# Performance work log

Measured on AMD Instinct MI355X. Metric: run time of the kernel, lower is better.

## Reference

```python
import jax, jax.numpy as jnp
import numpy as np

EMBED_DIM = 1024
NUM_HEADS = 16
HEAD_DIM = EMBED_DIM // NUM_HEADS
SPARSITY_LAMBDA = 0.01
B, S = 2, 2048


def setup_inputs() -> dict:
    key = jax.random.key(0)
    ks = jax.random.split(key, 10)
    scale = 0.02
    inp = {
        "x": jax.random.normal(ks[0], (B, S, EMBED_DIM), dtype=jnp.float32),
        "Wq": jax.random.normal(ks[1], (EMBED_DIM, EMBED_DIM), dtype=jnp.float32) * scale,
        "bq": jnp.zeros((EMBED_DIM,), dtype=jnp.float32),
        "Wk": jax.random.normal(ks[2], (EMBED_DIM, EMBED_DIM), dtype=jnp.float32) * scale,
        "bk": jnp.zeros((EMBED_DIM,), dtype=jnp.float32),
        "Wv": jax.random.normal(ks[3], (EMBED_DIM, EMBED_DIM), dtype=jnp.float32) * scale,
        "bv": jnp.zeros((EMBED_DIM,), dtype=jnp.float32),
        "Wo": jax.random.normal(ks[4], (EMBED_DIM, EMBED_DIM), dtype=jnp.float32) * scale,
        "bo": jnp.zeros((EMBED_DIM,), dtype=jnp.float32),
        "z": jax.random.normal(ks[5], (NUM_HEADS,), dtype=jnp.float32),
    }
    return inp


def reference(x, Wq, bq, Wk, bk, Wv, bv, Wo, bo, z):
    # Linear layers (torch Linear: y = x @ W.T + b); W here stored as [out, in]
    def split_heads(t):  # [B,S,E] -> [B,H,S,D]
        return t.reshape(B, S, NUM_HEADS, HEAD_DIM).transpose(0, 2, 1, 3)

    q = split_heads(x @ Wq.T + bq)
    k = split_heads(x @ Wk.T + bk)
    v = split_heads(x @ Wv.T + bv)

    scores = jnp.einsum("bhsd,bhtd->bhst", q, k) / jnp.sqrt(jnp.float32(HEAD_DIM))
    gate = jax.nn.sigmoid(z)  # [H], per-head scalar gate on raw scores
    scores = scores * gate[None, :, None, None]
    probs = jax.nn.softmax(scores, axis=-1)
    ctx = jnp.einsum("bhst,bhtd->bhsd", probs, v)  # [B,H,S,D]
    ctx = ctx.transpose(0, 2, 1, 3).reshape(B, S, EMBED_DIM)
    out = ctx @ Wo.T + bo
    penalty = jnp.sum(jax.nn.sigmoid(z)) * SPARSITY_LAMBDA
    return out, penalty
```

## Files before the change

kernel.cpp:

```cpp
#include <hip/hip_runtime.h>

typedef unsigned short ushort_t;
typedef __bf16 bf16x8 __attribute__((ext_vector_type(8)));
typedef ushort_t u16x8 __attribute__((ext_vector_type(8)));
typedef float f32x4 __attribute__((ext_vector_type(4)));
typedef unsigned int u32x2 __attribute__((ext_vector_type(2)));

#define DEVI __device__ __forceinline__

constexpr int Ed = 1024;
constexpr int Hh = 16;
constexpr int Dd = 64;
constexpr int Ss = 2048;
constexpr int Mm = 4096;

constexpr int NX4 = Mm * Ed / 4;
constexpr int NW4 = Ed * Ed / 4;

DEVI ushort_t f2bf(float f) {
    union { float f; unsigned int i; } v; v.f = f;
    unsigned int r = v.i + 0x7fffu + ((v.i >> 16) & 1u);
    return (ushort_t)(r >> 16);
}
DEVI ushort_t f2bf_hi(float f) {
    union { float f; unsigned int i; } v; v.f = f;
    return (ushort_t)(v.i >> 16);
}
DEVI unsigned int fbits(float f) {
    union { float f; unsigned int i; } v; v.f = f;
    return v.i;
}
DEVI float fast_exp2(float x) {
    float r;
    asm("v_exp_f32 %0, %1" : "=v"(r) : "v"(x));
    return r;
}

__global__ __launch_bounds__(256) void cvt_all(
    const float* __restrict__ x,  const float* __restrict__ Wq,
    const float* __restrict__ Wk, const float* __restrict__ Wv,
    const float* __restrict__ Wo,
    ushort_t* __restrict__ xb,  ushort_t* __restrict__ Wqb,
    ushort_t* __restrict__ Wkb, ushort_t* __restrict__ Wvb,
    ushort_t* __restrict__ Wob)
{
    int i = blockIdx.x * 256 + threadIdx.x;
    const float* s; ushort_t* d; int off;
    if (i < NX4)                { s = x;  d = xb;  off = i; }
    else if (i < NX4 + NW4)     { s = Wq; d = Wqb; off = i - NX4; }
    else if (i < NX4 + 2 * NW4) { s = Wk; d = Wkb; off = i - NX4 - NW4; }
    else if (i < NX4 + 3 * NW4) { s = Wv; d = Wvb; off = i - NX4 - 2 * NW4; }
    else                        { s = Wo; d = Wob; off = i - NX4 - 3 * NW4; }
    float4 v = ((const float4*)s)[off];
    ushort4 o; o.x = f2bf(v.x); o.y = f2bf(v.y); o.z = f2bf(v.z); o.w = f2bf(v.w);
    ((ushort4*)d)[off] = o;
}

DEVI void gld16(const void* g, void* l) {
    __builtin_amdgcn_global_load_lds(
        (__attribute__((address_space(1))) void*)(g),
        (__attribute__((address_space(3))) void*)(l), 16, 0, 0);
}

DEVI void gemm_core(const ushort_t* __restrict__ A, const ushort_t* __restrict__ W,
                    ushort_t* As, ushort_t* Bs, int tm, int tn, int K,
                    f32x4 acc[4][4])
{
    const int tid  = threadIdx.x;
    const int w    = tid >> 6;
    const int lane = tid & 63;
    const int quad = lane >> 4;
    const int l15  = lane & 15;
    const int wy   = w >> 1, wx = w & 1;
    const int rowc = lane >> 3;
    const int col8s = (((lane & 7) ^ rowc) * 8);
    const int swq  = l15 & 7;

    for (int k0 = 0; k0 < K; k0 += 64) {
        __syncthreads();
#pragma unroll
        for (int i = 0; i < 4; ++i) {
            int chunk = w * 4 + i;
            int row = chunk * 8 + rowc;
            gld16(A + (size_t)(tm + row) * K + k0 + col8s, (char*)As + chunk * 1024);
            gld16(W + (size_t)(tn + row) * K + k0 + col8s, (char*)Bs + chunk * 1024);
        }
        __syncthreads();
#pragma unroll
        for (int ks = 0; ks < 64; ks += 32) {
            const int k4 = ks >> 3;
            bf16x8 a[4], b[4];
#pragma unroll
            for (int mi = 0; mi < 4; ++mi)
                a[mi] = *(const bf16x8*)&As[(wy * 64 + mi * 16 + l15) * 64
                                            + (((quad + k4) ^ swq) * 8)];
#pragma unroll
            for (int ni = 0; ni < 4; ++ni)
                b[ni] = *(const bf16x8*)&Bs[(wx * 64 + ni * 16 + l15) * 64
                                            + (((quad + k4) ^ swq) * 8)];
#pragma unroll
            for (int mi = 0; mi < 4; ++mi)
#pragma unroll
                for (int ni = 0; ni < 4; ++ni)
                    acc[mi][ni] = __builtin_amdgcn_mfma_f32_16x16x32_bf16(
                        a[mi], b[ni], acc[mi][ni], 0, 0, 0);
        }
    }
}

__global__ __launch_bounds__(256, 3) void qkv_gemm(
    const ushort_t* __restrict__ x,
    const ushort_t* __restrict__ Wq, const float* __restrict__ bq,
    const ushort_t* __restrict__ Wk, const float* __restrict__ bk,
    const ushort_t* __restrict__ Wv, const float* __restrict__ bv,
    ushort_t* __restrict__ qo, ushort_t* __restrict__ ko, ushort_t* __restrict__ vto)
{
    __shared__ __align__(16) ushort_t As[128 * 64];
    __shared__ __align__(16) ushort_t Bs[128 * 64];
    const ushort_t* W; const float* bias; ushort_t* outp; int vmode;
    if (blockIdx.z == 0)      { W = Wq; bias = bq; outp = qo;  vmode = 0; }
    else if (blockIdx.z == 1) { W = Wk; bias = bk; outp = ko;  vmode = 0; }
    else                      { W = Wv; bias = bv; outp = vto; vmode = 1; }

    const int tm = blockIdx.x * 128, tn = blockIdx.y * 128;
    f32x4 acc[4][4] = {};
    gemm_core(x, W, As, Bs, tm, tn, Ed, acc);

    const int tid = threadIdx.x, w = tid >> 6, lane = tid & 63;
    const int quad = lane >> 4, l15 = lane & 15;
    const int wy = w >> 1, wx = w & 1;
    if (vmode == 0) {
#pragma unroll
        for (int ni = 0; ni < 4; ++ni) {
            int gc = tn + wx * 64 + ni * 16 + l15;
            float bb = bias[gc];
            int h = gc >> 6, d = gc & 63;
#pragma unroll
            for (int mi = 0; mi < 4; ++mi) {
#pragma unroll
                for (int r = 0; r < 4; ++r) {
                    int gr = tm + wy * 64 + mi * 16 + quad * 4 + r;
                    int b_ = gr >> 11, s_ = gr & 2047;
                    float v = acc[mi][ni][r] + bb;
                    outp[((size_t)(b_ * Hh + h) * Ss + s_) * Dd + d] = f2bf_hi(v);
                }
            }
        }
    } else {
#pragma unroll
        for (int ni = 0; ni < 4; ++ni) {
            int gc = tn + wx * 64 + ni * 16 + l15;
            float bb = bias[gc];
            int h = gc >> 6, d = gc & 63;
#pragma unroll
            for (int mi = 0; mi < 4; ++mi) {
                int gr0 = tm + wy * 64 + mi * 16 + quad * 4;
                int b_ = gr0 >> 11, s0 = gr0 & 2047;
                unsigned int u0 = fbits(acc[mi][ni][0] + bb);
                unsigned int u1 = fbits(acc[mi][ni][1] + bb);
                unsigned int u2 = fbits(acc[mi][ni][2] + bb);
                unsigned int u3 = fbits(acc[mi][ni][3] + bb);
                u32x2 pk;
                pk[0] = (u1 & 0xffff0000u) | (u0 >> 16);
                pk[1] = (u3 & 0xffff0000u) | (u2 >> 16);
                *(u32x2*)&outp[((size_t)(b_ * Hh + h) * Dd + d) * Ss + s0] = pk;
            }
        }
    }
}

__global__ __launch_bounds__(256, 3) void out_gemm(
    const ushort_t* __restrict__ ctx, const ushort_t* __restrict__ Wo,
    const float* __restrict__ bo, const float* __restrict__ z,
    float* __restrict__ out)
{
    __shared__ __align__(16) ushort_t As[128 * 64];
    __shared__ __align__(16) ushort_t Bs[64 * 64];
    const int tm = blockIdx.x * 128, tn = blockIdx.y * 64;

    const int tid  = threadIdx.x;
    const int w    = tid >> 6;
    const int lane = tid & 63;
    const int quad = lane >> 4;
    const int l15  = lane & 15;
    const int wy   = w >> 1, wx = w & 1;
    const int rowc = lane >> 3;
    const int col8s = (((lane & 7) ^ rowc) * 8);
    const int swq  = l15 & 7;

    f32x4 acc[4][2] = {};
    for (int k0 = 0; k0 < Ed; k0 += 64) {
        __syncthreads();
#pragma unroll
        for (int i = 0; i < 4; ++i) {
            int chunk = w * 4 + i;
            int row = chunk * 8 + rowc;
            gld16(ctx + (size_t)(tm + row) * Ed + k0 + col8s, (char*)As + chunk * 1024);
        }
#pragma unroll
        for (int i = 0; i < 2; ++i) {
            int chunk = w * 2 + i;
            int row = chunk * 8 + rowc;
            gld16(Wo + (size_t)(tn + row) * Ed + k0 + col8s, (char*)Bs + chunk * 1024);
        }
        __syncthreads();
#pragma unroll
        for (int ks = 0; ks < 64; ks += 32) {
            const int k4 = ks >> 3;
            bf16x8 a[4], b[2];
#pragma unroll
            for (int mi = 0; mi < 4; ++mi)
                a[mi] = *(const bf16x8*)&As[(wy * 64 + mi * 16 + l15) * 64
                                            + (((quad + k4) ^ swq) * 8)];
#pragma unroll
            for (int ni = 0; ni < 2; ++ni)
                b[ni] = *(const bf16x8*)&Bs[(wx * 32 + ni * 16 + l15) * 64
                                            + (((quad + k4) ^ swq) * 8)];
#pragma unroll
            for (int mi = 0; mi < 4; ++mi)
#pragma unroll
                for (int ni = 0; ni < 2; ++ni)
                    acc[mi][ni] = __builtin_amdgcn_mfma_f32_16x16x32_bf16(
                        a[mi], b[ni], acc[mi][ni], 0, 0, 0);
        }
    }

#pragma unroll
    for (int ni = 0; ni < 2; ++ni) {
        int gc = tn + wx * 32 + ni * 16 + l15;
        float bb = bo[gc];
#pragma unroll
        for (int mi = 0; mi < 4; ++mi)
#pragma unroll
            for (int r = 0; r < 4; ++r) {
                int gr = tm + wy * 64 + mi * 16 + quad * 4 + r;
                out[(size_t)gr * Ed + gc] = acc[mi][ni][r] + bb;
            }
    }

    if (blockIdx.x == 0 && blockIdx.y == 0 && tid == 0) {
        float s = 0.f;
        for (int hh = 0; hh < Hh; ++hh) s += 1.f / (1.f + __expf(-z[hh]));
        out[(size_t)Mm * Ed] = s * 0.01f;
    }
}

__global__ __launch_bounds__(256, 2) void attn(
    const ushort_t* __restrict__ Q, const ushort_t* __restrict__ Kk,
    const ushort_t* __restrict__ Vt, const float* __restrict__ z,
    ushort_t* __restrict__ ctx)
{
    __shared__ __align__(16) ushort_t Ks[2][128 * 64];
    __shared__ __align__(16) ushort_t Ps[4][32 * 68];

    const int tid = threadIdx.x, w = tid >> 6, lane = tid & 63;
    const int quad = lane >> 4, l15 = lane & 15;
    const int lin = blockIdx.x + 16 * blockIdx.y;
    const int qt = lin >> 5;
    const int bh = (lin & 7) * 4 + ((lin >> 3) & 3);
    const int h = bh & (Hh - 1), b_ = bh >> 4;
    const size_t base = (size_t)bh * Ss * Dd;

    const float gate = 1.f / (1.f + __expf(-z[h]));
    const float scl2 = gate * 0.125f * 1.44269504f;

    bf16x8 aQ[2][2];
#pragma unroll
    for (int m = 0; m < 2; ++m)
#pragma unroll
        for (int c = 0; c < 2; ++c)
            aQ[m][c] = *(const bf16x8*)&Q[base
                + (size_t)(qt * 128 + w * 32 + m * 16 + l15) * Dd + c * 32 + quad * 8];

    const int rowc = lane >> 3;
    const int gs   = ((lane & 7) ^ rowc) * 8;
    const ushort_t* kSrc[4];
#pragma unroll
    for (int i = 0; i < 4; ++i)
        kSrc[i] = Kk + base + (size_t)(w * 32 + i * 8 + rowc) * Dd + gs;
    const ushort_t* vBase = Vt + base + (size_t)l15 * Ss + quad * 8;

    f32x4 accO[2][4] = {};
    float lsum[2][4] = {};

    const int swq = (l15 & 7) * 8;

#pragma unroll
    for (int i = 0; i < 4; ++i)
        gld16(kSrc[i], (char*)Ks[0] + (w * 4 + i) * 1024);

    for (int kt = 0; kt < Ss / 128; ++kt) {
        const int cur = kt & 1, nxt = cur ^ 1;
        __syncthreads();

        if (kt + 1 < Ss / 128) {
#pragma unroll
            for (int i = 0; i < 4; ++i)
                gld16(kSrc[i] + (size_t)(kt + 1) * 128 * Dd,
                      (char*)Ks[nxt] + (w * 4 + i) * 1024);
        }

#pragma unroll
        for (int sub = 0; sub < 2; ++sub) {
            bf16x8 vf[2][4];
#pragma unroll
            for (int ni = 0; ni < 4; ++ni) {
                const ushort_t* vp = vBase + (size_t)(ni * 16) * Ss + kt * 128 + sub * 64;
                vf[0][ni] = *(const bf16x8*)(vp);
                vf[1][ni] = *(const bf16x8*)(vp + 32);
            }

            f32x4 sAcc[2][4] = {};
            __builtin_amdgcn_s_setprio(1);
#pragma unroll
            for (int ni = 0; ni < 4; ++ni) {
                bf16x8 b0 = *(const bf16x8*)&Ks[cur][(sub * 64 + ni * 16 + l15) * 64 + ((quad * 8) ^ swq)];
                bf16x8 b1 = *(const bf16x8*)&Ks[cur][(sub * 64 + ni * 16 + l15) * 64 + (((quad + 4) * 8) ^ swq)];
#pragma unroll
                for (int m = 0; m < 2; ++m) {
                    sAcc[m][ni] = __builtin_amdgcn_mfma_f32_16x16x32_bf16(aQ[m][0], b0, sAcc[m][ni], 0, 0, 0);
                    sAcc[m][ni] = __builtin_amdgcn_mfma_f32_16x16x32_bf16(aQ[m][1], b1, sAcc[m][ni], 0, 0, 0);
                }
            }
            __builtin_amdgcn_s_setprio(0);

#pragma unroll
            for (int m = 0; m < 2; ++m)
#pragma unroll
                for (int ni = 0; ni < 4; ++ni)
#pragma unroll
                    for (int r = 0; r < 4; ++r) {
                        float p = fast_exp2(sAcc[m][ni][r] * scl2);
                        lsum[m][r] += p;
                        Ps[w][(m * 16 + quad * 4 + r) * 68 + ni * 16 + l15] = f2bf_hi(p);
                    }

            __builtin_amdgcn_s_setprio(1);
#pragma unroll
            for (int c = 0; c < 2; ++c) {
                bf16x8 aP0 = *(const bf16x8*)&Ps[w][l15 * 68 + c * 32 + quad * 8];
                bf16x8 aP1 = *(const bf16x8*)&Ps[w][(16 + l15) * 68 + c * 32 + quad * 8];
#pragma unroll
                for (int ni = 0; ni < 4; ++ni) {
                    accO[0][ni] = __builtin_amdgcn_mfma_f32_16x16x32_bf16(aP0, vf[c][ni], accO[0][ni], 0, 0, 0);
                    accO[1][ni] = __builtin_amdgcn_mfma_f32_16x16x32_bf16(aP1, vf[c][ni], accO[1][ni], 0, 0, 0);
                }
            }
            __builtin_amdgcn_s_setprio(0);
        }
    }

#pragma unroll
    for (int m = 0; m < 2; ++m)
#pragma unroll
        for (int r = 0; r < 4; ++r) {
            lsum[m][r] += __shfl_xor(lsum[m][r], 1);
            lsum[m][r] += __shfl_xor(lsum[m][r], 2);
            lsum[m][r] += __shfl_xor(lsum[m][r], 4);
            lsum[m][r] += __shfl_xor(lsum[m][r], 8);
        }

#pragma unroll
    for (int m = 0; m < 2; ++m)
#pragma unroll
        for (int r = 0; r < 4; ++r) {
            int srow = qt * 128 + w * 32 + m * 16 + quad * 4 + r;
            float inv = 1.f / lsum[m][r];
#pragma unroll
            for (int ni = 0; ni < 4; ++ni) {
                int d = ni * 16 + l15;
                ctx[((size_t)(b_ * Ss + srow)) * Ed + h * Dd + d] = f2bf_hi(accO[m][ni][r] * inv);
            }
        }
}

extern "C" void kernel_launch(void* const* d_in, const int* in_sizes, int n_in,
                              void* d_out, int out_size, void* d_ws, size_t ws_size,
                              hipStream_t stream) {
    const float* x  = (const float*)d_in[0];
    const float* Wq = (const float*)d_in[1];
    const float* bq = (const float*)d_in[2];
    const float* Wk = (const float*)d_in[3];
    const float* bk = (const float*)d_in[4];
    const float* Wv = (const float*)d_in[5];
    const float* bv = (const float*)d_in[6];
    const float* Wo = (const float*)d_in[7];
    const float* bo = (const float*)d_in[8];
    const float* z  = (const float*)d_in[9];
    float* out = (float*)d_out;

    ushort_t* xb  = (ushort_t*)d_ws;
    ushort_t* Wqb = xb  + (size_t)Mm * Ed;
    ushort_t* Wkb = Wqb + (size_t)Ed * Ed;
    ushort_t* Wvb = Wkb + (size_t)Ed * Ed;
    ushort_t* Wob = Wvb + (size_t)Ed * Ed;
    ushort_t* qw  = Wob + (size_t)Ed * Ed;
    ushort_t* kw  = qw + (size_t)Mm * Ed;
    ushort_t* vT  = kw + (size_t)Mm * Ed;
    ushort_t* cx  = vT + (size_t)Mm * Ed;

    dim3 blk(256);
    cvt_all<<<dim3((NX4 + 4 * NW4) / 256), blk, 0, stream>>>(
        x, Wq, Wk, Wv, Wo, xb, Wqb, Wkb, Wvb, Wob);
    qkv_gemm<<<dim3(Mm / 128, Ed / 128, 3), blk, 0, stream>>>(
        xb, Wqb, bq, Wkb, bk, Wvb, bv, qw, kw, vT);
    attn<<<dim3(Ss / 128, 2 * Hh), blk, 0, stream>>>(qw, kw, vT, z, cx);
    out_gemm<<<dim3(Mm / 128, Ed / 64), blk, 0, stream>>>(cx, Wob, bo, z, out);
}
```

Baseline: 209.6 us.

## Load K fragments directly into registers instead of LDS double buffering

Drops the shared-memory K tile and its per-iteration __syncthreads. Each wave now loads its K MFMA operands straight from global memory into registers, using a register ping-pong (kfA/kfB) that prefetches the next half-tile while the current one computes. This removes LDS traffic and block-wide barriers, but each wave now reads K on its own, which raises global/L2 traffic by four times and adds register pressure at the 2-waves launch bound.

```diff
diff --git a/kernel.cpp b/kernel.cpp
--- a/kernel.cpp
+++ b/kernel.cpp
@@ -250,7 +250,6 @@
     const ushort_t* __restrict__ Vt, const float* __restrict__ z,
     ushort_t* __restrict__ ctx)
 {
-    __shared__ __align__(16) ushort_t Ks[2][128 * 64];
     __shared__ __align__(16) ushort_t Ps[4][32 * 68];
 
     const int tid = threadIdx.x, w = tid >> 6, lane = tid & 63;
@@ -272,56 +271,98 @@
             aQ[m][c] = *(const bf16x8*)&Q[base
                 + (size_t)(qt * 128 + w * 32 + m * 16 + l15) * Dd + c * 32 + quad * 8];
 
-    const int rowc = lane >> 3;
-    const int gs   = ((lane & 7) ^ rowc) * 8;
-    const ushort_t* kSrc[4];
-#pragma unroll
-    for (int i = 0; i < 4; ++i)
-        kSrc[i] = Kk + base + (size_t)(w * 32 + i * 8 + rowc) * Dd + gs;
+    const ushort_t* kBase = Kk + base + (size_t)l15 * Dd + quad * 8;
     const ushort_t* vBase = Vt + base + (size_t)l15 * Ss + quad * 8;
 
     f32x4 accO[2][4] = {};
     float lsum[2][4] = {};
 
-    const int swq = (l15 & 7) * 8;
-
-#pragma unroll
-    for (int i = 0; i < 4; ++i)
-        gld16(kSrc[i], (char*)Ks[0] + (w * 4 + i) * 1024);
-
+    bf16x8 kfA[8], kfB[8];
+#pragma unroll
+    for (int ni = 0; ni < 4; ++ni) {
+        const ushort_t* p = kBase + (size_t)(ni * 16) * Dd;
+        kfA[ni * 2 + 0] = *(const bf16x8*)(p);
+        kfA[ni * 2 + 1] = *(const bf16x8*)(p + 32);
+    }
+
+#pragma unroll 1
     for (int kt = 0; kt < Ss / 128; ++kt) {
-        const int cur = kt & 1, nxt = cur ^ 1;
-        __syncthreads();
-
-        if (kt + 1 < Ss / 128) {
-#pragma unroll
-            for (int i = 0; i < 4; ++i)
-                gld16(kSrc[i] + (size_t)(kt + 1) * 128 * Dd,
-                      (char*)Ks[nxt] + (w * 4 + i) * 1024);
-        }
-
-#pragma unroll
-        for (int sub = 0; sub < 2; ++sub) {
+        {
             bf16x8 vf[2][4];
 #pragma unroll
             for (int ni = 0; ni < 4; ++ni) {
-                const ushort_t* vp = vBase + (size_t)(ni * 16) * Ss + kt * 128 + sub * 64;
+                const ushort_t* vp = vBase + (size_t)(ni * 16) * Ss + kt * 128;
                 vf[0][ni] = *(const bf16x8*)(vp);
                 vf[1][ni] = *(const bf16x8*)(vp + 32);
             }
+#pragma unroll
+            for (int ni = 0; ni < 4; ++ni) {
+                const ushort_t* p = kBase + (size_t)(kt * 128 + 64 + ni * 16) * Dd;
+                kfB[ni * 2 + 0] = *(const bf16x8*)(p);
+                kfB[ni * 2 + 1] = *(const bf16x8*)(p + 32);
+            }
 
             f32x4 sAcc[2][4] = {};
             __builtin_amdgcn_s_setprio(1);
 #pragma unroll
+            for (int ni = 0; ni < 4; ++ni)
+#pragma unroll
+                for (int m = 0; m < 2; ++m) {
+                    sAcc[m][ni] = __builtin_amdgcn_mfma_f32_16x16x32_bf16(aQ[m][0], kfA[ni * 2 + 0], sAcc[m][ni], 0, 0, 0);
+                    sAcc[m][ni] = __builtin_amdgcn_mfma_f32_16x16x32_bf16(aQ[m][1], kfA[ni * 2 + 1], sAcc[m][ni], 0, 0, 0);
+                }
+            __builtin_amdgcn_s_setprio(0);
+
+#pragma unroll
+            for (int m = 0; m < 2; ++m)
+#pragma unroll
+                for (int ni = 0; ni < 4; ++ni)
+#pragma unroll
+                    for (int r = 0; r < 4; ++r) {
+                        float p = fast_exp2(sAcc[m][ni][r] * scl2);
+                        lsum[m][r] += p;
+                        Ps[w][(m * 16 + quad * 4 + r) * 68 + ni * 16 + l15] = f2bf_hi(p);
+                    }
+
+            __builtin_amdgcn_s_setprio(1);
+#pragma unroll
+            for (int c = 0; c < 2; ++c) {
+                bf16x8 aP0 = *(const bf16x8*)&Ps[w][l15 * 68 + c * 32 + quad * 8];
+                bf16x8 aP1 = *(const bf16x8*)&Ps[w][(16 + l15) * 68 + c * 32 + quad * 8];
+#pragma unroll
+                for (int ni = 0; ni < 4; ++ni) {
+                    accO[0][ni] = __builtin_amdgcn_mfma_f32_16x16x32_bf16(aP0, vf[c][ni], accO[0][ni], 0, 0, 0);
+                    accO[1][ni] = __builtin_amdgcn_mfma_f32_16x16x32_bf16(aP1, vf[c][ni], accO[1][ni], 0, 0, 0);
+                }
+            }
+            __builtin_amdgcn_s_setprio(0);
+        }
+        {
+            bf16x8 vf[2][4];
+#pragma unroll
             for (int ni = 0; ni < 4; ++ni) {
-                bf16x8 b0 = *(const bf16x8*)&Ks[cur][(sub * 64 + ni * 16 + l15) * 64 + ((quad * 8) ^ swq)];
-                bf16x8 b1 = *(const bf16x8*)&Ks[cur][(sub * 64 + ni * 16 + l15) * 64 + (((quad + 4) * 8) ^ swq)];
+                const ushort_t* vp = vBase + (size_t)(ni * 16) * Ss + kt * 128 + 64;
+                vf[0][ni] = *(const bf16x8*)(vp);
+                vf[1][ni] = *(const bf16x8*)(vp + 32);
+            }
+            if (kt + 1 < Ss / 128) {
+#pragma unroll
+                for (int ni = 0; ni < 4; ++ni) {
+                    const ushort_t* p = kBase + (size_t)((kt + 1) * 128 + ni * 16) * Dd;
+                    kfA[ni * 2 + 0] = *(const bf16x8*)(p);
+                    kfA[ni * 2 + 1] = *(const bf16x8*)(p + 32);
+                }
+            }
+
+            f32x4 sAcc[2][4] = {};
+            __builtin_amdgcn_s_setprio(1);
+#pragma unroll
+            for (int ni = 0; ni < 4; ++ni)
 #pragma unroll
                 for (int m = 0; m < 2; ++m) {
-                    sAcc[m][ni] = __builtin_amdgcn_mfma_f32_16x16x32_bf16(aQ[m][0], b0, sAcc[m][ni], 0, 0, 0);
-                    sAcc[m][ni] = __builtin_amdgcn_mfma_f32_16x16x32_bf16(aQ[m][1], b1, sAcc[m][ni], 0, 0, 0);
-                }
-            }
+                    sAcc[m][ni] = __builtin_amdgcn_mfma_f32_16x16x32_bf16(aQ[m][0], kfB[ni * 2 + 0], sAcc[m][ni], 0, 0, 0);
+                    sAcc[m][ni] = __builtin_amdgcn_mfma_f32_16x16x32_bf16(aQ[m][1], kfB[ni * 2 + 1], sAcc[m][ni], 0, 0, 0);
+                }
             __builtin_amdgcn_s_setprio(0);
 
 #pragma unroll
```

Measured after the change: 255.6 us. +22.0%, slower.

## Software-pipeline attention sub-tiles so QK MFMA overlaps softmax exp of previous half

Applied to the files above, without the earlier changes.

The two 64-key sub-tiles of each 128-key K block are manually unrolled and reordered. The second QK^T product is issued before the first PV product, and the second exp/convert runs after that PV. The P scratch buffer is doubled per wave so the two halves do not collide. The goal is to overlap MFMA work with the VALU exp and LDS traffic, at the cost of more live registers (two score accumulators) and extra LDS.

```diff
diff --git a/kernel.cpp b/kernel.cpp
--- a/kernel.cpp
+++ b/kernel.cpp
@@ -251,7 +251,7 @@
     ushort_t* __restrict__ ctx)
 {
     __shared__ __align__(16) ushort_t Ks[2][128 * 64];
-    __shared__ __align__(16) ushort_t Ps[4][32 * 68];
+    __shared__ __align__(16) ushort_t Ps[4][2][32 * 68];
 
     const int tid = threadIdx.x, w = tid >> 6, lane = tid & 63;
     const int quad = lane >> 4, l15 = lane & 15;
@@ -300,54 +300,97 @@
                       (char*)Ks[nxt] + (w * 4 + i) * 1024);
         }
 
-#pragma unroll
-        for (int sub = 0; sub < 2; ++sub) {
-            bf16x8 vf[2][4];
+        bf16x8 vf0[2][4];
+#pragma unroll
+        for (int ni = 0; ni < 4; ++ni) {
+            const ushort_t* vp = vBase + (size_t)(ni * 16) * Ss + kt * 128;
+            vf0[0][ni] = *(const bf16x8*)(vp);
+            vf0[1][ni] = *(const bf16x8*)(vp + 32);
+        }
+
+        f32x4 s0[2][4] = {};
+        __builtin_amdgcn_s_setprio(1);
+#pragma unroll
+        for (int ni = 0; ni < 4; ++ni) {
+            bf16x8 b0 = *(const bf16x8*)&Ks[cur][(ni * 16 + l15) * 64 + ((quad * 8) ^ swq)];
+            bf16x8 b1 = *(const bf16x8*)&Ks[cur][(ni * 16 + l15) * 64 + (((quad + 4) * 8) ^ swq)];
+#pragma unroll
+            for (int m = 0; m < 2; ++m) {
+                s0[m][ni] = __builtin_amdgcn_mfma_f32_16x16x32_bf16(aQ[m][0], b0, s0[m][ni], 0, 0, 0);
+                s0[m][ni] = __builtin_amdgcn_mfma_f32_16x16x32_bf16(aQ[m][1], b1, s0[m][ni], 0, 0, 0);
+            }
+        }
+        __builtin_amdgcn_s_setprio(0);
+
+#pragma unroll
+        for (int m = 0; m < 2; ++m)
+#pragma unroll
+            for (int ni = 0; ni < 4; ++ni)
+#pragma unroll
+                for (int r = 0; r < 4; ++r) {
+                    float p = fast_exp2(s0[m][ni][r] * scl2);
+                    lsum[m][r] += p;
+                    Ps[w][0][(m * 16 + quad * 4 + r) * 68 + ni * 16 + l15] = f2bf_hi(p);
+                }
+
+        f32x4 s1[2][4] = {};
+        __builtin_amdgcn_s_setprio(1);
+#pragma unroll
+        for (int ni = 0; ni < 4; ++ni) {
+            bf16x8 b0 = *(const bf16x8*)&Ks[cur][(64 + ni * 16 + l15) * 64 + ((quad * 8) ^ swq)];
+            bf16x8 b1 = *(const bf16x8*)&Ks[cur][(64 + ni * 16 + l15) * 64 + (((quad + 4) * 8) ^ swq)];
+#pragma unroll
+            for (int m = 0; m < 2; ++m) {
+                s1[m][ni] = __builtin_amdgcn_mfma_f32_16x16x32_bf16(aQ[m][0], b0, s1[m][ni], 0, 0, 0);
+                s1[m][ni] = __builtin_amdgcn_mfma_f32_16x16x32_bf16(aQ[m][1], b1, s1[m][ni], 0, 0, 0);
+            }
+        }
+        __builtin_amdgcn_s_setprio(0);
+
+        bf16x8 vf1[2][4];
+#pragma unroll
+        for (int ni = 0; ni < 4; ++ni) {
+            const ushort_t* vp = vBase + (size_t)(ni * 16) * Ss + kt * 128 + 64;
+            vf1[0][ni] = *(const bf16x8*)(vp);
+            vf1[1][ni] = *(const bf16x8*)(vp + 32);
+        }
+
+        __builtin_amdgcn_s_setprio(1);
+#pragma unroll
+        for (int c = 0; c < 2; ++c) {
+            bf16x8 aP0 = *(const bf16x8*)&Ps[w][0][l15 * 68 + c * 32 + quad * 8];
+            bf16x8 aP1 = *(const bf16x8*)&Ps[w][0][(16 + l15) * 68 + c * 32 + quad * 8];
 #pragma unroll
             for (int ni = 0; ni < 4; ++ni) {
-                const ushort_t* vp = vBase + (size_t)(ni * 16) * Ss + kt * 128 + sub * 64;
-                vf[0][ni] = *(const bf16x8*)(vp);
-                vf[1][ni] = *(const bf16x8*)(vp + 32);
-            }
-
-            f32x4 sAcc[2][4] = {};
-            __builtin_amdgcn_s_setprio(1);
+                accO[0][ni] = __builtin_amdgcn_mfma_f32_16x16x32_bf16(aP0, vf0[c][ni], accO[0][ni], 0, 0, 0);
+                accO[1][ni] = __builtin_amdgcn_mfma_f32_16x16x32_bf16(aP1, vf0[c][ni], accO[1][ni], 0, 0, 0);
+            }
+        }
+        __builtin_amdgcn_s_setprio(0);
+
+#pragma unroll
+        for (int m = 0; m < 2; ++m)
+#pragma unroll
+            for (int ni = 0; ni < 4; ++ni)
+#pragma unroll
+                for (int r = 0; r < 4; ++r) {
+                    float p = fast_exp2(s1[m][ni][r] * scl2);
+                    lsum[m][r] += p;
+                    Ps[w][1][(m * 16 + quad * 4 + r) * 68 + ni * 16 + l15] = f2bf_hi(p);
+                }
+
+        __builtin_amdgcn_s_setprio(1);
+#pragma unroll
+        for (int c = 0; c < 2; ++c) {
+            bf16x8 aP0 = *(const bf16x8*)&Ps[w][1][l15 * 68 + c * 32 + quad * 8];
+            bf16x8 aP1 = *(const bf16x8*)&Ps[w][1][(16 + l15) * 68 + c * 32 + quad * 8];
 #pragma unroll
             for (int ni = 0; ni < 4; ++ni) {
-                bf16x8 b0 = *(const bf16x8*)&Ks[cur][(sub * 64 + ni * 16 + l15) * 64 + ((quad * 8) ^ swq)];
-                bf16x8 b1 = *(const bf16x8*)&Ks[cur][(sub * 64 + ni * 16 + l15) * 64 + (((quad + 4) * 8) ^ swq)];
-#pragma unroll
-                for (int m = 0; m < 2; ++m) {
-                    sAcc[m][ni] = __builtin_amdgcn_mfma_f32_16x16x32_bf16(aQ[m][0], b0, sAcc[m][ni], 0, 0, 0);
-                    sAcc[m][ni] = __builtin_amdgcn_mfma_f32_16x16x32_bf16(aQ[m][1], b1, sAcc[m][ni], 0, 0, 0);
-                }
-            }
-            __builtin_amdgcn_s_setprio(0);
-
-#pragma unroll
-            for (int m = 0; m < 2; ++m)
-#pragma unroll
-                for (int ni = 0; ni < 4; ++ni)
-#pragma unroll
-                    for (int r = 0; r < 4; ++r) {
-                        float p = fast_exp2(sAcc[m][ni][r] * scl2);
-                        lsum[m][r] += p;
-                        Ps[w][(m * 16 + quad * 4 + r) * 68 + ni * 16 + l15] = f2bf_hi(p);
-                    }
-
-            __builtin_amdgcn_s_setprio(1);
-#pragma unroll
-            for (int c = 0; c < 2; ++c) {
-                bf16x8 aP0 = *(const bf16x8*)&Ps[w][l15 * 68 + c * 32 + quad * 8];
-                bf16x8 aP1 = *(const bf16x8*)&Ps[w][(16 + l15) * 68 + c * 32 + quad * 8];
-#pragma unroll
-                for (int ni = 0; ni < 4; ++ni) {
-                    accO[0][ni] = __builtin_amdgcn_mfma_f32_16x16x32_bf16(aP0, vf[c][ni], accO[0][ni], 0, 0, 0);
-                    accO[1][ni] = __builtin_amdgcn_mfma_f32_16x16x32_bf16(aP1, vf[c][ni], accO[1][ni], 0, 0, 0);
-                }
-            }
-            __builtin_amdgcn_s_setprio(0);
-        }
+                accO[0][ni] = __builtin_amdgcn_mfma_f32_16x16x32_bf16(aP0, vf1[c][ni], accO[0][ni], 0, 0, 0);
+                accO[1][ni] = __builtin_amdgcn_mfma_f32_16x16x32_bf16(aP1, vf1[c][ni], accO[1][ni], 0, 0, 0);
+            }
+        }
+        __builtin_amdgcn_s_setprio(0);
     }
 
 #pragma unroll
```

Measured after the change: 217.3 us. 1.04x slower.

## Compute transposed scores to keep P in registers and drop LDS round-trip

Applied to the files above, without the earlier changes.

The attention kernel now computes S^T by swapping the MFMA operands (K as A, Q as B). The exponentiated probabilities then land in the register layout that a 16x16x16 bf16 MFMA expects for its B operand, so P·V runs directly from registers and the per-wave LDS scratch buffer is gone. V fragments are loaded as 4-element vectors, row sums need only two cross-lane shuffles, and ctx is written as packed 4-element stores. The trade-off is twice as many, smaller MFMAs for P·V (16x16x16 instead of 16x16x32), narrower global V loads, and more live registers for the V fragments.

```diff
diff --git a/kernel.cpp b/kernel.cpp
--- a/kernel.cpp
+++ b/kernel.cpp
@@ -5,6 +5,7 @@
 typedef ushort_t u16x8 __attribute__((ext_vector_type(8)));
 typedef float f32x4 __attribute__((ext_vector_type(4)));
 typedef unsigned int u32x2 __attribute__((ext_vector_type(2)));
+typedef short s16x4 __attribute__((ext_vector_type(4)));
 
 #define DEVI __device__ __forceinline__
 
@@ -34,6 +35,22 @@
     float r;
     asm("v_exp_f32 %0, %1" : "=v"(r) : "v"(x));
     return r;
+}
+DEVI unsigned int pkbf(float lo, float hi) {
+    return (fbits(hi) & 0xffff0000u) | (fbits(lo) >> 16);
+}
+
+DEVI f32x4 mfma16(s16x4 a, s16x4 b, f32x4 c) {
+#if __has_builtin(__builtin_amdgcn_mfma_f32_16x16x16bf16_1k)
+    return __builtin_amdgcn_mfma_f32_16x16x16bf16_1k(a, b, c, 0, 0, 0);
+#elif __has_builtin(__builtin_amdgcn_mfma_f32_16x16x16_bf16_1k)
+    return __builtin_amdgcn_mfma_f32_16x16x16_bf16_1k(a, b, c, 0, 0, 0);
+#else
+    f32x4 d = c;
+    asm volatile("v_mfma_f32_16x16x16_bf16 %0, %1, %2, %0"
+                 : "+v"(d) : "v"(a), "v"(b));
+    return d;
+#endif
 }
 
 __global__ __launch_bounds__(256) void cvt_all(
@@ -156,13 +173,9 @@
             for (int mi = 0; mi < 4; ++mi) {
                 int gr0 = tm + wy * 64 + mi * 16 + quad * 4;
                 int b_ = gr0 >> 11, s0 = gr0 & 2047;
-                unsigned int u0 = fbits(acc[mi][ni][0] + bb);
-                unsigned int u1 = fbits(acc[mi][ni][1] + bb);
-                unsigned int u2 = fbits(acc[mi][ni][2] + bb);
-                unsigned int u3 = fbits(acc[mi][ni][3] + bb);
                 u32x2 pk;
-                pk[0] = (u1 & 0xffff0000u) | (u0 >> 16);
-                pk[1] = (u3 & 0xffff0000u) | (u2 >> 16);
+                pk[0] = pkbf(acc[mi][ni][0] + bb, acc[mi][ni][1] + bb);
+                pk[1] = pkbf(acc[mi][ni][2] + bb, acc[mi][ni][3] + bb);
                 *(u32x2*)&outp[((size_t)(b_ * Hh + h) * Dd + d) * Ss + s0] = pk;
             }
         }
@@ -251,7 +264,6 @@
     ushort_t* __restrict__ ctx)
 {
     __shared__ __align__(16) ushort_t Ks[2][128 * 64];
-    __shared__ __align__(16) ushort_t Ps[4][32 * 68];
 
     const int tid = threadIdx.x, w = tid >> 6, lane = tid & 63;
     const int quad = lane >> 4, l15 = lane & 15;
@@ -278,10 +290,10 @@
 #pragma unroll
     for (int i = 0; i < 4; ++i)
         kSrc[i] = Kk + base + (size_t)(w * 32 + i * 8 + rowc) * Dd + gs;
-    const ushort_t* vBase = Vt + base + (size_t)l15 * Ss + quad * 8;
+    const ushort_t* vBase = Vt + base + (size_t)l15 * Ss + quad * 4;
 
     f32x4 accO[2][4] = {};
-    float lsum[2][4] = {};
+    float lsum[2] = {0.f, 0.f};
 
     const int swq = (l15 & 7) * 8;
 
@@ -302,76 +314,77 @@
 
 #pragma unroll
         for (int sub = 0; sub < 2; ++sub) {
-            bf16x8 vf[2][4];
+            const int key0 = kt * 128 + sub * 64;
+
+            s16x4 vf16[4][4];
+#pragma unroll
+            for (int kc = 0; kc < 4; ++kc)
+#pragma unroll
+                for (int ni = 0; ni < 4; ++ni)
+                    vf16[kc][ni] = *(const s16x4*)(vBase + (size_t)(ni * 16) * Ss
+                                                   + key0 + kc * 16);
+
+            f32x4 sT[2][4] = {};
+            __builtin_amdgcn_s_setprio(1);
 #pragma unroll
             for (int ni = 0; ni < 4; ++ni) {
-                const ushort_t* vp = vBase + (size_t)(ni * 16) * Ss + kt * 128 + sub * 64;
-                vf[0][ni] = *(const bf16x8*)(vp);
-                vf[1][ni] = *(const bf16x8*)(vp + 32);
-            }
-
-            f32x4 sAcc[2][4] = {};
-            __builtin_amdgcn_s_setprio(1);
-#pragma unroll
-            for (int ni = 0; ni < 4; ++ni) {
-                bf16x8 b0 = *(const bf16x8*)&Ks[cur][(sub * 64 + ni * 16 + l15) * 64 + ((quad * 8) ^ swq)];
-                bf16x8 b1 = *(const bf16x8*)&Ks[cur][(sub * 64 + ni * 16 + l15) * 64 + (((quad + 4) * 8) ^ swq)];
+                bf16x8 k0f = *(const bf16x8*)&Ks[cur][(sub * 64 + ni * 16 + l15) * 64 + ((quad * 8) ^ swq)];
+                bf16x8 k1f = *(const bf16x8*)&Ks[cur][(sub * 64 + ni * 16 + l15) * 64 + (((quad + 4) * 8) ^ swq)];
 #pragma unroll
                 for (int m = 0; m < 2; ++m) {
-                    sAcc[m][ni] = __builtin_amdgcn_mfma_f32_16x16x32_bf16(aQ[m][0], b0, sAcc[m][ni], 0, 0, 0);
-                    sAcc[m][ni] = __builtin_amdgcn_mfma_f32_16x16x32_bf16(aQ[m][1], b1, sAcc[m][ni], 0, 0, 0);
+                    sT[m][ni] = __builtin_amdgcn_mfma_f32_16x16x32_bf16(k0f, aQ[m][0], sT[m][ni], 0, 0, 0);
+                    sT[m][ni] = __builtin_amdgcn_mfma_f32_16x16x32_bf16(k1f, aQ[m][1], sT[m][ni], 0, 0, 0);
                 }
             }
             __builtin_amdgcn_s_setprio(0);
 
+            s16x4 pb[2][4];
 #pragma unroll
             for (int m = 0; m < 2; ++m)
 #pragma unroll
-                for (int ni = 0; ni < 4; ++ni)
-#pragma unroll
-                    for (int r = 0; r < 4; ++r) {
-                        float p = fast_exp2(sAcc[m][ni][r] * scl2);
-                        lsum[m][r] += p;
-                        Ps[w][(m * 16 + quad * 4 + r) * 68 + ni * 16 + l15] = f2bf_hi(p);
-                    }
+                for (int ni = 0; ni < 4; ++ni) {
+                    float p0 = fast_exp2(sT[m][ni][0] * scl2);
+                    float p1 = fast_exp2(sT[m][ni][1] * scl2);
+                    float p2 = fast_exp2(sT[m][ni][2] * scl2);
+                    float p3 = fast_exp2(sT[m][ni][3] * scl2);
+                    lsum[m] += (p0 + p1) + (p2 + p3);
+                    union { unsigned int u[2]; s16x4 v; } uu;
+                    uu.u[0] = pkbf(p0, p1);
+                    uu.u[1] = pkbf(p2, p3);
+                    pb[m][ni] = uu.v;
+                }
 
             __builtin_amdgcn_s_setprio(1);
 #pragma unroll
-            for (int c = 0; c < 2; ++c) {
-                bf16x8 aP0 = *(const bf16x8*)&Ps[w][l15 * 68 + c * 32 + quad * 8];
-                bf16x8 aP1 = *(const bf16x8*)&Ps[w][(16 + l15) * 68 + c * 32 + quad * 8];
-#pragma unroll
-                for (int ni = 0; ni < 4; ++ni) {
-                    accO[0][ni] = __builtin_amdgcn_mfma_f32_16x16x32_bf16(aP0, vf[c][ni], accO[0][ni], 0, 0, 0);
-                    accO[1][ni] = __builtin_amdgcn_mfma_f32_16x16x32_bf16(aP1, vf[c][ni], accO[1][ni], 0, 0, 0);
-                }
-            }
+            for (int kc = 0; kc < 4; ++kc)
+#pragma unroll
+                for (int m = 0; m < 2; ++m)
+#pragma unroll
+                    for (int ni = 0; ni < 4; ++ni)
+                        accO[m][ni] = mfma16(vf16[kc][ni], pb[m][kc], accO[m][ni]);
             __builtin_amdgcn_s_setprio(0);
         }
     }
 
 #pragma unroll
-    for (int m = 0; m < 2; ++m)
-#pragma unroll
-        for (int r = 0; r < 4; ++r) {
-            lsum[m][r] += __shfl_xor(lsum[m][r], 1);
-            lsum[m][r] += __shfl_xor(lsum[m][r], 2);
-            lsum[m][r] += __shfl_xor(lsum[m][r], 4);
-            lsum[m][r] += __shfl_xor(lsum[m][r], 8);
-        }
-
-#pragma unroll
-    for (int m = 0; m < 2; ++m)
-#pragma unroll
-        for (int r = 0; r < 4; ++r) {
-            int srow = qt * 128 + w * 32 + m * 16 + quad * 4 + r;
-            float inv = 1.f / lsum[m][r];
-#pragma unroll
-            for (int ni = 0; ni < 4; ++ni) {
-                int d = ni * 16 + l15;
-                ctx[((size_t)(b_ * Ss + srow)) * Ed + h * Dd + d] = f2bf_hi(accO[m][ni][r] * inv);
-            }
-        }
+    for (int m = 0; m < 2; ++m) {
+        lsum[m] += __shfl_xor(lsum[m], 16);
+        lsum[m] += __shfl_xor(lsum[m], 32);
+    }
+
+#pragma unroll
+    for (int m = 0; m < 2; ++m) {
+        int srow = qt * 128 + w * 32 + m * 16 + l15;
+        float inv = 1.f / lsum[m];
+        ushort_t* crow = ctx + ((size_t)(b_ * Ss + srow)) * Ed + h * Dd + quad * 4;
+#pragma unroll
+        for (int ni = 0; ni < 4; ++ni) {
+            u32x2 pk;
+            pk[0] = pkbf(accO[m][ni][0] * inv, accO[m][ni][1] * inv);
+            pk[1] = pkbf(accO[m][ni][2] * inv, accO[m][ni][3] * inv);
+            *(u32x2*)&crow[ni * 16] = pk;
+        }
+    }
 }
 
 extern "C" void kernel_launch(void* const* d_in, const int* in_sizes, int n_in,
```

New measurement: 264.9 us. 1.26x slower.
